# Performance work log

Hardware: AMD Instinct MI355X
Metric: run time of the kernel (lower is better)

The kernel has to match this reference:

```python
import jax, jax.numpy as jnp
import numpy as np

LAMB = 0.5  # penalty coefficient (init kwarg lamb)


def setup_inputs() -> dict:
    key = jax.random.key(0)
    k1, k2, k3 = jax.random.split(key, 3)
    B, T, D, K = 4, 512, 256, 512
    reps = jax.random.normal(k1, (B, T, D), jnp.float32)
    rep_table = jax.random.normal(k2, (B, T, T, D), jnp.float32)
    centers = jax.random.normal(k3, (K, D), jnp.float32)
    return {"reps": reps, "rep_table": rep_table, "centers": centers, "timestep": T}


def reference(reps, rep_table, centers, timestep):
    B, T, D = reps.shape
    t = timestep  # min(max_len, timestep) with max_len=1e9
    dtype = reps.dtype

    # ~mask after torch.flip: row i keeps columns j >= t-1-i  (segment length i+1)
    keep = (jnp.arange(t)[None, :] >= (t - 1 - jnp.arange(t))[:, None]).astype(dtype)
    seg_lengths = jnp.arange(t, dtype=dtype) + 1.0  # (t,)

    # masked segment sum over dim 2, then average: (B, t, D)
    x = jnp.einsum('ij,bijd->bid', keep, rep_table[:, :t, :t]) / seg_lengths[None, :, None]

    # codebook attention: softmax(x C^T / sqrt(D)) C  -> (B, t, D)
    scale = 1.0 / jnp.sqrt(jnp.asarray(D, dtype))
    attn = jax.nn.softmax(jnp.einsum('bid,kd->bik', x, centers) * scale, axis=-1)
    xa = jnp.einsum('bik,kd->bid', attn, centers)

    # L2 distance to each center, expanded form to avoid (B,t,K,D) tensor
    l2 = (jnp.sum(xa * xa, axis=-1)[:, :, None]
          - 2.0 * jnp.einsum('bid,kd->bik', xa, centers)
          + jnp.sum(centers * centers, axis=-1)[None, None, :])  # (B, t, K)

    loss = l2 + (LAMB * (1.0 - seg_lengths))[None, :, None]

    val = jnp.min(loss, axis=2)      # (B, t)
    idxs = jnp.argmin(loss, axis=2)  # (B, t)

    costs = jnp.full((B, T + 1), jnp.inf, dtype).at[:, :t].set(val[:, ::-1])
    tokens = jnp.zeros((B, T + 1), jnp.int32).at[:, :t].set(idxs[:, ::-1].astype(jnp.int32))
    return costs, tokens
```

## Files before the change

kernel.cpp:

```cpp
#include <hip/hip_runtime.h>
#include <math.h>
#include <float.h>

#define TT 512
#define DD 256
#define KK 512
#define LAMBDA 0.5f

typedef float f4 __attribute__((ext_vector_type(4)));

__device__ __forceinline__ f4 ntload(const f4* p) {
    return __builtin_nontemporal_load(p);
}

__device__ __forceinline__ void fma4(f4& a, float s, f4 c) {
    a.x = fmaf(s, c.x, a.x);
    a.y = fmaf(s, c.y, a.y);
    a.z = fmaf(s, c.z, a.z);
    a.w = fmaf(s, c.w, a.w);
}

__device__ __forceinline__ unsigned short f2bf(float f) {
    unsigned int u = __float_as_uint(f);
    unsigned int r = (u + 0x7FFFu + ((u >> 16) & 1u)) >> 16;
    return (unsigned short)r;
}

__global__ __launch_bounds__(256) void seg_mean_kernel(const float* __restrict__ tbl,
                                                       float* __restrict__ x) {
    const int blk = blockIdx.x;
    const int b = blk >> 8;
    const int p = blk & 255;
    const int i0 = p;
    const int i1 = TT - 1 - p;
    const int tid = threadIdx.x;
    const int jj = tid >> 6;
    const int d4 = tid & 63;

    const f4* __restrict__ base0 =
        (const f4*)tbl + (size_t)(b * TT + i0) * (TT * (DD / 4));
    const f4* __restrict__ base1 =
        (const f4*)tbl + (size_t)(b * TT + i1) * (TT * (DD / 4));

    f4 accA = (f4)(0.f), accB = (f4)(0.f);
    {
        int j = TT - 1 - p + jj;
        for (; j + 4 < TT; j += 8) {
            f4 v0 = ntload(base0 + (size_t)j * 64 + d4);
            f4 v1 = ntload(base0 + (size_t)(j + 4) * 64 + d4);
            accA += v0; accB += v1;
        }
        if (j < TT) accA += ntload(base0 + (size_t)j * 64 + d4);
    }
    f4 acc0 = accA + accB;
    accA = (f4)(0.f); accB = (f4)(0.f);
    {
        int j = p + jj;
        for (; j + 4 < TT; j += 8) {
            f4 v0 = ntload(base1 + (size_t)j * 64 + d4);
            f4 v1 = ntload(base1 + (size_t)(j + 4) * 64 + d4);
            accA += v0; accB += v1;
        }
        if (j < TT) accA += ntload(base1 + (size_t)j * 64 + d4);
    }
    f4 acc1 = accA + accB;

    __shared__ f4 red0[4][64];
    __shared__ f4 red1[4][64];
    red0[jj][d4] = acc0;
    red1[jj][d4] = acc1;
    __syncthreads();
    if (tid < 128) {
        const int r = tid >> 6;
        const int d = tid & 63;
        const f4 (*red)[64] = r ? red1 : red0;
        const int i = r ? i1 : i0;
        f4 o = (red[0][d] + red[1][d]) + (red[2][d] + red[3][d]);
        o *= 0.0625f / (float)(i + 1);
        ((f4*)(x + (size_t)(b * TT + i) * DD))[d] = o;
    }
}

__global__ __launch_bounds__(256) void prep_kernel(const float* __restrict__ C,
                                                   float* __restrict__ CT,
                                                   float* __restrict__ cn2) {
    const int blk = blockIdx.x;
    const int tid = threadIdx.x;
    if (blk < 32) {
        __shared__ float tile[64][65];
        const int k0 = (blk & 7) * 64;
        const int d0 = (blk >> 3) * 64;
        const int kk = tid >> 4;
        const int dl = (tid & 15) * 4;
#pragma unroll
        for (int r = 0; r < 4; ++r) {
            const float4 v = *(const float4*)&C[(size_t)(k0 + kk + r * 16) * DD + d0 + dl];
            tile[kk + r * 16][dl + 0] = v.x;
            tile[kk + r * 16][dl + 1] = v.y;
            tile[kk + r * 16][dl + 2] = v.z;
            tile[kk + r * 16][dl + 3] = v.w;
        }
        __syncthreads();
        const int dd = tid >> 4;
        const int kl = (tid & 15) * 4;
#pragma unroll
        for (int r = 0; r < 4; ++r) {
            const int d = dd + r * 16;
            float4 o = make_float4(tile[kl + 0][d], tile[kl + 1][d],
                                   tile[kl + 2][d], tile[kl + 3][d]);
            *(float4*)&CT[(size_t)(d0 + d) * KK + k0 + kl] = o;
        }
    } else {
        const int w = tid >> 6, lane = tid & 63;
        const int k = (blk - 32) * 4 + w;
        const float4 v = *(const float4*)&C[(size_t)k * DD + lane * 4];
        float s = v.x * v.x + v.y * v.y + v.z * v.z + v.w * v.w;
#pragma unroll
        for (int off = 32; off > 0; off >>= 1) s += __shfl_xor(s, off, 64);
        if (lane == 0) cn2[k] = s;
    }
}

__global__ __launch_bounds__(512) void attn_argmin_kernel(
        const float* __restrict__ x, const float* __restrict__ C,
        const float* __restrict__ CT, const float* __restrict__ cn2,
        unsigned short* __restrict__ out, int Btot) {
    __shared__ char part_raw[65536];
    f4 (*scpart)[8][128] = (f4 (*)[8][128])part_raw;
    f4 (*xpart)[8][64]   = (f4 (*)[8][64])part_raw;
    __shared__ float xs[8][DD];
    __shared__ float sc[8][KK];
    __shared__ float xav[8][DD];
    __shared__ float rinv[8];
    __shared__ float xn2s[8];

    const int tid = threadIdx.x;
    const int lane = tid & 63;
    const int wv = tid >> 6;
    const int row0 = blockIdx.x * 8;

    ((f4*)&xs[0][0])[tid] = ((const f4*)(x + (size_t)row0 * DD))[tid];
    __syncthreads();

    {
        const int g = tid >> 7;
        const int k4 = tid & 127;
        const f4* CTv = (const f4*)CT + (size_t)(g * 64) * (KK / 4) + k4;
        f4 acc[8];
#pragma unroll
        for (int r = 0; r < 8; ++r) acc[r] = (f4)(0.f);
        for (int dd = 0; dd < 64; ++dd) {
            f4 c = CTv[dd * (KK / 4)];
            const int d = g * 64 + dd;
#pragma unroll
            for (int r = 0; r < 8; ++r) fma4(acc[r], xs[r][d], c);
        }
#pragma unroll
        for (int r = 0; r < 8; ++r) scpart[g][r][k4] = acc[r];
    }
    __syncthreads();
    {
#pragma unroll
        for (int it = 0; it < 2; ++it) {
            const int idx = tid * 2 + it;
            const int row = idx >> 7, k4 = idx & 127;
            f4 s = (scpart[0][row][k4] + scpart[1][row][k4])
                 + (scpart[2][row][k4] + scpart[3][row][k4]);
            ((f4*)sc[row])[k4] = s;
        }
    }
    __syncthreads();

    {
        const int r = wv;
        float v[8];
        float m = -INFINITY;
#pragma unroll
        for (int q = 0; q < 8; ++q) {
            v[q] = sc[r][lane + 64 * q];
            m = fmaxf(m, v[q]);
        }
#pragma unroll
        for (int off = 32; off > 0; off >>= 1) m = fmaxf(m, __shfl_xor(m, off, 64));
        float ssum = 0.f;
#pragma unroll
        for (int q = 0; q < 8; ++q) {
            float e = expf(v[q] - m);
            sc[r][lane + 64 * q] = e;
            ssum += e;
        }
#pragma unroll
        for (int off = 32; off > 0; off >>= 1) ssum += __shfl_xor(ssum, off, 64);
        if (lane == 0) rinv[r] = 1.f / ssum;
    }
    __syncthreads();

    {
        const int kb = wv * 64;
        const f4* Cv = (const f4*)C + (size_t)kb * (DD / 4) + lane;
        f4 acc[8];
#pragma unroll
        for (int r = 0; r < 8; ++r) acc[r] = (f4)(0.f);
        for (int kk = 0; kk < 64; ++kk) {
            f4 c = Cv[kk * (DD / 4)];
            const int k = kb + kk;
#pragma unroll
            for (int r = 0; r < 8; ++r) fma4(acc[r], sc[r][k], c);
        }
#pragma unroll
        for (int r = 0; r < 8; ++r) xpart[wv][r][lane] = acc[r];
    }
    __syncthreads();
    {
        const int row = wv, d4 = lane;
        f4 s = ((xpart[0][row][d4] + xpart[1][row][d4])
              + (xpart[2][row][d4] + xpart[3][row][d4]))
             + ((xpart[4][row][d4] + xpart[5][row][d4])
              + (xpart[6][row][d4] + xpart[7][row][d4]));
        s *= rinv[row];
        ((f4*)xav[row])[d4] = s;
        float n = s.x * s.x + s.y * s.y + s.z * s.z + s.w * s.w;
#pragma unroll
        for (int off = 32; off > 0; off >>= 1) n += __shfl_xor(n, off, 64);
        if (lane == 0) xn2s[row] = n;
    }
    __syncthreads();

    {
        const int g = tid >> 7;
        const int k4 = tid & 127;
        const f4* CTv = (const f4*)CT + (size_t)(g * 64) * (KK / 4) + k4;
        f4 acc[8];
#pragma unroll
        for (int r = 0; r < 8; ++r) acc[r] = (f4)(0.f);
        for (int dd = 0; dd < 64; ++dd) {
            f4 c = CTv[dd * (KK / 4)];
            const int d = g * 64 + dd;
#pragma unroll
            for (int r = 0; r < 8; ++r) fma4(acc[r], xav[r][d], c);
        }
#pragma unroll
        for (int r = 0; r < 8; ++r) scpart[g][r][k4] = acc[r];
    }
    __syncthreads();
    {
        float mv = FLT_MAX;
        int mi = 0;
#pragma unroll
        for (int it = 0; it < 2; ++it) {
            const int idx = tid * 2 + it;
            const int k4 = idx & 127;
            f4 dot = (scpart[0][wv][k4] + scpart[1][wv][k4])
                   + (scpart[2][wv][k4] + scpart[3][wv][k4]);
            f4 cn = ((const f4*)cn2)[k4];
            float l0 = cn.x - 2.f * dot.x;
            float l1 = cn.y - 2.f * dot.y;
            float l2 = cn.z - 2.f * dot.z;
            float l3 = cn.w - 2.f * dot.w;
            float lv = l0; int li = k4 * 4;
            if (l1 < lv) { lv = l1; li = k4 * 4 + 1; }
            if (l2 < lv) { lv = l2; li = k4 * 4 + 2; }
            if (l3 < lv) { lv = l3; li = k4 * 4 + 3; }
            if (lv < mv || (lv == mv && li < mi)) { mv = lv; mi = li; }
        }
#pragma unroll
        for (int off = 32; off > 0; off >>= 1) {
            float ov = __shfl_xor(mv, off, 64);
            int oi = __shfl_xor(mi, off, 64);
            if (ov < mv || (ov == mv && oi < mi)) { mv = ov; mi = oi; }
        }
        if (lane == 0) {
            const int row = row0 + wv;
            const int b = row >> 9;
            const int i = row & (TT - 1);
            const float pen = LAMBDA * (1.f - (float)(i + 1));
            const float val = mv + xn2s[wv] + pen;
            out[b * (TT + 1) + (TT - 1 - i)] = f2bf(val);
            out[Btot * (TT + 1) + b * (TT + 1) + (TT - 1 - i)] = f2bf((float)mi);
        }
    }
    if (tid == 511 && (row0 & (TT - 1)) == 0) {
        const int b = row0 >> 9;
        out[b * (TT + 1) + TT] = 0x7F7F;
        out[Btot * (TT + 1) + b * (TT + 1) + TT] = 0;
    }
}

extern "C" void kernel_launch(void* const* d_in, const int* in_sizes, int n_in,
                              void* d_out, int out_size, void* d_ws, size_t ws_size,
                              hipStream_t stream) {
    const float* rep_table = (const float*)d_in[1];
    const float* centers   = (const float*)d_in[2];
    unsigned short* out = (unsigned short*)d_out;

    const int Btot = in_sizes[0] / (TT * DD);

    float* x   = (float*)d_ws;
    float* CT  = x + (size_t)Btot * TT * DD;
    float* cn2 = CT + (size_t)DD * KK;

    prep_kernel<<<160, 256, 0, stream>>>(centers, CT, cn2);
    seg_mean_kernel<<<Btot * (TT / 2), 256, 0, stream>>>(rep_table, x);
    attn_argmin_kernel<<<(Btot * TT) / 8, 512, 0, stream>>>(x, centers, CT, cn2,
                                                            out, Btot);
}
```

Measured before the change: 113.0 us.

## Fuse segment-mean reduction into attention/argmin kernel with 4 rows per block

```diff
diff --git a/kernel.cpp b/kernel.cpp
--- a/kernel.cpp
+++ b/kernel.cpp
@@ -24,61 +24,6 @@
     unsigned int u = __float_as_uint(f);
     unsigned int r = (u + 0x7FFFu + ((u >> 16) & 1u)) >> 16;
     return (unsigned short)r;
-}
-
-__global__ __launch_bounds__(256) void seg_mean_kernel(const float* __restrict__ tbl,
-                                                       float* __restrict__ x) {
-    const int blk = blockIdx.x;
-    const int b = blk >> 8;
-    const int p = blk & 255;
-    const int i0 = p;
-    const int i1 = TT - 1 - p;
-    const int tid = threadIdx.x;
-    const int jj = tid >> 6;
-    const int d4 = tid & 63;
-
-    const f4* __restrict__ base0 =
-        (const f4*)tbl + (size_t)(b * TT + i0) * (TT * (DD / 4));
-    const f4* __restrict__ base1 =
-        (const f4*)tbl + (size_t)(b * TT + i1) * (TT * (DD / 4));
-
-    f4 accA = (f4)(0.f), accB = (f4)(0.f);
-    {
-        int j = TT - 1 - p + jj;
-        for (; j + 4 < TT; j += 8) {
-            f4 v0 = ntload(base0 + (size_t)j * 64 + d4);
-            f4 v1 = ntload(base0 + (size_t)(j + 4) * 64 + d4);
-            accA += v0; accB += v1;
-        }
-        if (j < TT) accA += ntload(base0 + (size_t)j * 64 + d4);
-    }
-    f4 acc0 = accA + accB;
-    accA = (f4)(0.f); accB = (f4)(0.f);
-    {
-        int j = p + jj;
-        for (; j + 4 < TT; j += 8) {
-            f4 v0 = ntload(base1 + (size_t)j * 64 + d4);
-            f4 v1 = ntload(base1 + (size_t)(j + 4) * 64 + d4);
-            accA += v0; accB += v1;
-        }
-        if (j < TT) accA += ntload(base1 + (size_t)j * 64 + d4);
-    }
-    f4 acc1 = accA + accB;
-
-    __shared__ f4 red0[4][64];
-    __shared__ f4 red1[4][64];
-    red0[jj][d4] = acc0;
-    red1[jj][d4] = acc1;
-    __syncthreads();
-    if (tid < 128) {
-        const int r = tid >> 6;
-        const int d = tid & 63;
-        const f4 (*red)[64] = r ? red1 : red0;
-        const int i = r ? i1 : i0;
-        f4 o = (red[0][d] + red[1][d]) + (red[2][d] + red[3][d]);
-        o *= 0.0625f / (float)(i + 1);
-        ((f4*)(x + (size_t)(b * TT + i) * DD))[d] = o;
-    }
 }
 
 __global__ __launch_bounds__(256) void prep_kernel(const float* __restrict__ C,
@@ -121,57 +66,94 @@
     }
 }
 
-__global__ __launch_bounds__(512) void attn_argmin_kernel(
-        const float* __restrict__ x, const float* __restrict__ C,
+__global__ __launch_bounds__(512) void fused_kernel(
+        const float* __restrict__ tbl, const float* __restrict__ C,
         const float* __restrict__ CT, const float* __restrict__ cn2,
         unsigned short* __restrict__ out, int Btot) {
-    __shared__ char part_raw[65536];
-    f4 (*scpart)[8][128] = (f4 (*)[8][128])part_raw;
-    f4 (*xpart)[8][64]   = (f4 (*)[8][64])part_raw;
-    __shared__ float xs[8][DD];
-    __shared__ float sc[8][KK];
-    __shared__ float xav[8][DD];
-    __shared__ float rinv[8];
-    __shared__ float xn2s[8];
+    __shared__ char part_raw[32768];
+    f4 (*red)[4][64]     = (f4 (*)[4][64])part_raw;
+    f4 (*scpart)[4][128] = (f4 (*)[4][128])part_raw;
+    f4 (*xpart)[4][64]   = (f4 (*)[4][64])part_raw;
+    __shared__ float xs[4][DD];
+    __shared__ float sc[4][KK];
+    __shared__ float xav[4][DD];
+    __shared__ float rinv[4];
+    __shared__ float xn2s[4];
 
     const int tid = threadIdx.x;
     const int lane = tid & 63;
     const int wv = tid >> 6;
-    const int row0 = blockIdx.x * 8;
-
-    ((f4*)&xs[0][0])[tid] = ((const f4*)(x + (size_t)row0 * DD))[tid];
+    const int blk = blockIdx.x;
+    const int b = blk >> 7;
+    const int pg = blk & 127;
+    const int pP[2] = { pg, pg + 128 };
+
+    {
+        const int q = wv >> 2;
+        const int jj = wv & 3;
+        const int p = pP[q];
+        const f4* baseS = (const f4*)tbl + (size_t)(b * TT + p) * (TT * (DD / 4));
+        const f4* baseL = (const f4*)tbl + (size_t)(b * TT + (TT - 1 - p)) * (TT * (DD / 4));
+        f4 aA = (f4)(0.f), aB = (f4)(0.f);
+        {
+            int j = p + jj;
+            for (; j + 4 < TT; j += 8) {
+                f4 v0 = ntload(baseL + (size_t)j * 64 + lane);
+                f4 v1 = ntload(baseL + (size_t)(j + 4) * 64 + lane);
+                aA += v0; aB += v1;
+            }
+            if (j < TT) aA += ntload(baseL + (size_t)j * 64 + lane);
+        }
+        red[2 * q + 1][jj][lane] = aA + aB;
+        aA = (f4)(0.f); aB = (f4)(0.f);
+        {
+            int j = TT - 1 - p + jj;
+            for (; j + 4 < TT; j += 8) {
+                f4 v0 = ntload(baseS + (size_t)j * 64 + lane);
+                f4 v1 = ntload(baseS + (size_t)(j + 4) * 64 + lane);
+                aA += v0; aB += v1;
+            }
+            if (j < TT) aA += ntload(baseS + (size_t)j * 64 + lane);
+        }
+        red[2 * q][jj][lane] = aA + aB;
+    }
+    __syncthreads();
+    if (tid < 256) {
+        const int r = tid >> 6;
+        const int d = tid & 63;
+        const int p = pP[r >> 1];
+        const int m = (r & 1) ? (TT - p) : (p + 1);
+        f4 s = (red[r][0][d] + red[r][1][d]) + (red[r][2][d] + red[r][3][d]);
+        s *= 0.0625f / (float)m;
+        ((f4*)xs[r])[d] = s;
+    }
     __syncthreads();
 
     {
         const int g = tid >> 7;
         const int k4 = tid & 127;
         const f4* CTv = (const f4*)CT + (size_t)(g * 64) * (KK / 4) + k4;
-        f4 acc[8];
-#pragma unroll
-        for (int r = 0; r < 8; ++r) acc[r] = (f4)(0.f);
+        f4 acc[4];
+#pragma unroll
+        for (int r = 0; r < 4; ++r) acc[r] = (f4)(0.f);
         for (int dd = 0; dd < 64; ++dd) {
             f4 c = CTv[dd * (KK / 4)];
             const int d = g * 64 + dd;
 #pragma unroll
-            for (int r = 0; r < 8; ++r) fma4(acc[r], xs[r][d], c);
-        }
-#pragma unroll
-        for (int r = 0; r < 8; ++r) scpart[g][r][k4] = acc[r];
-    }
-    __syncthreads();
-    {
-#pragma unroll
-        for (int it = 0; it < 2; ++it) {
-            const int idx = tid * 2 + it;
-            const int row = idx >> 7, k4 = idx & 127;
-            f4 s = (scpart[0][row][k4] + scpart[1][row][k4])
-                 + (scpart[2][row][k4] + scpart[3][row][k4]);
-            ((f4*)sc[row])[k4] = s;
-        }
-    }
-    __syncthreads();
-
-    {
+            for (int r = 0; r < 4; ++r) fma4(acc[r], xs[r][d], c);
+        }
+#pragma unroll
+        for (int r = 0; r < 4; ++r) scpart[g][r][k4] = acc[r];
+    }
+    __syncthreads();
+    {
+        const int row = tid >> 7, k4 = tid & 127;
+        ((f4*)sc[row])[k4] = (scpart[0][row][k4] + scpart[1][row][k4])
+                           + (scpart[2][row][k4] + scpart[3][row][k4]);
+    }
+    __syncthreads();
+
+    if (wv < 4) {
         const int r = wv;
         float v[8];
         float m = -INFINITY;
@@ -198,21 +180,21 @@
     {
         const int kb = wv * 64;
         const f4* Cv = (const f4*)C + (size_t)kb * (DD / 4) + lane;
-        f4 acc[8];
-#pragma unroll
-        for (int r = 0; r < 8; ++r) acc[r] = (f4)(0.f);
+        f4 acc[4];
+#pragma unroll
+        for (int r = 0; r < 4; ++r) acc[r] = (f4)(0.f);
         for (int kk = 0; kk < 64; ++kk) {
             f4 c = Cv[kk * (DD / 4)];
             const int k = kb + kk;
 #pragma unroll
-            for (int r = 0; r < 8; ++r) fma4(acc[r], sc[r][k], c);
-        }
-#pragma unroll
-        for (int r = 0; r < 8; ++r) xpart[wv][r][lane] = acc[r];
-    }
-    __syncthreads();
-    {
-        const int row = wv, d4 = lane;
+            for (int r = 0; r < 4; ++r) fma4(acc[r], sc[r][k], c);
+        }
+#pragma unroll
+        for (int r = 0; r < 4; ++r) xpart[wv][r][lane] = acc[r];
+    }
+    __syncthreads();
+    if (tid < 256) {
+        const int row = tid >> 6, d4 = tid & 63;
         f4 s = ((xpart[0][row][d4] + xpart[1][row][d4])
               + (xpart[2][row][d4] + xpart[3][row][d4]))
              + ((xpart[4][row][d4] + xpart[5][row][d4])
@@ -222,7 +204,7 @@
         float n = s.x * s.x + s.y * s.y + s.z * s.z + s.w * s.w;
 #pragma unroll
         for (int off = 32; off > 0; off >>= 1) n += __shfl_xor(n, off, 64);
-        if (lane == 0) xn2s[row] = n;
+        if (d4 == 0) xn2s[row] = n;
     }
     __syncthreads();
 
@@ -230,26 +212,26 @@
         const int g = tid >> 7;
         const int k4 = tid & 127;
         const f4* CTv = (const f4*)CT + (size_t)(g * 64) * (KK / 4) + k4;
-        f4 acc[8];
-#pragma unroll
-        for (int r = 0; r < 8; ++r) acc[r] = (f4)(0.f);
+        f4 acc[4];
+#pragma unroll
+        for (int r = 0; r < 4; ++r) acc[r] = (f4)(0.f);
         for (int dd = 0; dd < 64; ++dd) {
             f4 c = CTv[dd * (KK / 4)];
             const int d = g * 64 + dd;
 #pragma unroll
-            for (int r = 0; r < 8; ++r) fma4(acc[r], xav[r][d], c);
-        }
-#pragma unroll
-        for (int r = 0; r < 8; ++r) scpart[g][r][k4] = acc[r];
-    }
-    __syncthreads();
-    {
+            for (int r = 0; r < 4; ++r) fma4(acc[r], xav[r][d], c);
+        }
+#pragma unroll
+        for (int r = 0; r < 4; ++r) scpart[g][r][k4] = acc[r];
+    }
+    __syncthreads();
+
+    if (wv < 4) {
         float mv = FLT_MAX;
         int mi = 0;
 #pragma unroll
         for (int it = 0; it < 2; ++it) {
-            const int idx = tid * 2 + it;
-            const int k4 = idx & 127;
+            const int k4 = lane + 64 * it;
             f4 dot = (scpart[0][wv][k4] + scpart[1][wv][k4])
                    + (scpart[2][wv][k4] + scpart[3][wv][k4]);
             f4 cn = ((const f4*)cn2)[k4];
@@ -270,17 +252,15 @@
             if (ov < mv || (ov == mv && oi < mi)) { mv = ov; mi = oi; }
         }
         if (lane == 0) {
-            const int row = row0 + wv;
-            const int b = row >> 9;
-            const int i = row & (TT - 1);
+            const int p = pP[wv >> 1];
+            const int i = (wv & 1) ? (TT - 1 - p) : p;
             const float pen = LAMBDA * (1.f - (float)(i + 1));
             const float val = mv + xn2s[wv] + pen;
             out[b * (TT + 1) + (TT - 1 - i)] = f2bf(val);
             out[Btot * (TT + 1) + b * (TT + 1) + (TT - 1 - i)] = f2bf((float)mi);
         }
     }
-    if (tid == 511 && (row0 & (TT - 1)) == 0) {
-        const int b = row0 >> 9;
+    if (tid == 511 && pg == 0) {
         out[b * (TT + 1) + TT] = 0x7F7F;
         out[Btot * (TT + 1) + b * (TT + 1) + TT] = 0;
     }
@@ -295,12 +275,10 @@
 
     const int Btot = in_sizes[0] / (TT * DD);
 
-    float* x   = (float*)d_ws;
-    float* CT  = x + (size_t)Btot * TT * DD;
+    float* CT  = (float*)d_ws;
     float* cn2 = CT + (size_t)DD * KK;
 
     prep_kernel<<<160, 256, 0, stream>>>(centers, CT, cn2);
-    seg_mean_kernel<<<Btot * (TT / 2), 256, 0, stream>>>(rep_table, x);
-    attn_argmin_kernel<<<(Btot * TT) / 8, 512, 0, stream>>>(x, centers, CT, cn2,
-                                                            out, Btot);
-}
+    fused_kernel<<<Btot * (TT / 4), 512, 0, stream>>>(rep_table, centers, CT,
+                                                      cn2, out, Btot);
+}
```

After: 116.0 us. +2.7%, slower.
